# Optimization experiments

Hardware: AMD Instinct MI355X
Metric: run time of the kernel (lower is better)

## Reference

```python
import jax, jax.numpy as jnp
import numpy as np

B, S, D = 2, 1024, 2048      # batch, seq_len, hidden
H, HD = 16, 128              # heads, head_dim
FF = 8192                    # SwiGLU intermediate
R = 3                        # num_recursion
NEG = -1e9                   # additive mask fill (finfo.min analogue)
TEMP, ALPHA = 1.0, 1.0


def _rmsnorm(x, w, eps=1e-6):
    return x * jax.lax.rsqrt(jnp.mean(x * x, axis=-1, keepdims=True) + eps) * w


def _rot_half(x):
    x1, x2 = jnp.split(x, 2, axis=-1)
    return jnp.concatenate([-x2, x1], axis=-1)


def _block(x, cos, sin, sel, ln1, ln2, Wq, Wk, Wv, Wo, Wg, Wu, Wd):
    # Llama decoder layer restricted to selected tokens.
    # The torch code gathers selected tokens + their rows/cols of the 4D causal
    # mask + their RoPE embeddings, runs dense attention on the packed subset,
    # then scatters back. That is mathematically identical to dense attention
    # over the full sequence where keys are masked to selected tokens and only
    # selected-query outputs are kept (RoPE uses ORIGINAL positions in both).
    b, s, d = x.shape
    h = _rmsnorm(x, ln1)
    q = (h @ Wq).reshape(b, s, H, HD)
    k = (h @ Wk).reshape(b, s, H, HD)
    v = (h @ Wv).reshape(b, s, H, HD)
    cs = cos[None, :, None, :]
    sn = sin[None, :, None, :]
    q = q * cs + _rot_half(q) * sn
    k = k * cs + _rot_half(k) * sn
    scores = jnp.einsum('bqhd,bkhd->bhqk', q, k) / np.float32(np.sqrt(HD))
    causal = jnp.tril(jnp.ones((s, s), dtype=bool))
    allowed = causal[None, None, :, :] & sel[:, None, None, :]  # key must be selected
    attn = jax.nn.softmax(jnp.where(allowed, scores, NEG), axis=-1)
    o = jnp.einsum('bhqk,bkhd->bqhd', attn, v).reshape(b, s, d) @ Wo
    x = x + o
    h2 = _rmsnorm(x, ln2)
    return x + (jax.nn.silu(h2 @ Wg) * (h2 @ Wu)) @ Wd


def setup_inputs() -> dict:
    key = jax.random.key(0)
    ks = jax.random.split(key, 9)
    x = jax.random.normal(ks[0], (B, S, D), dtype=jnp.float32)
    # RoPE tables at original positions (what position_embeddings carries)
    inv_freq = 1.0 / (10000.0 ** (np.arange(0, HD, 2, dtype=np.float32) / HD))
    freqs = np.outer(np.arange(S, dtype=np.float32), inv_freq)
    emb = np.concatenate([freqs, freqs], axis=-1)
    cos = jnp.asarray(np.cos(emb), dtype=jnp.float32)
    sin = jnp.asarray(np.sin(emb), dtype=jnp.float32)
    sc = 0.02
    p = lambda k, shp: jax.random.normal(k, shp, dtype=jnp.float32) * sc
    return dict(
        x=x, cos=cos, sin=sin,
        w_router=p(ks[1], (D, R)),
        ln1=jnp.ones((D,), dtype=jnp.float32),
        ln2=jnp.ones((D,), dtype=jnp.float32),
        Wq=p(ks[2], (D, D)), Wk=p(ks[3], (D, D)),
        Wv=p(ks[4], (D, D)), Wo=p(ks[5], (D, D)),
        Wg=p(ks[6], (D, FF)), Wu=p(ks[7], (D, FF)), Wd=p(ks[8], (FF, D)),
    )


def reference(x, cos, sin, w_router, ln1, ln2, Wq, Wk, Wv, Wo, Wg, Wu, Wd):
    # token-level MoR routing: top-1 depth per token, token at depth r is
    # processed by blocks 0..r and its (weighted) output at depth r is final.
    probs = jax.nn.softmax((x / TEMP) @ w_router, axis=-1) * ALPHA  # [B,S,R]
    top_idx = jnp.argmax(probs, axis=-1)                            # [B,S]
    w = jnp.take_along_axis(probs, top_idx[..., None], axis=-1)     # [B,S,1]
    final_x = x
    cur = x
    for index in range(R):
        sel = top_idx >= index                                      # tokens still active
        out = _block(cur, cos, sin, sel, ln1, ln2, Wq, Wk, Wv, Wo, Wg, Wu, Wd)
        fin = (top_idx == index)[..., None]
        final_x = jnp.where(fin, out * w, final_x)                  # finished: scatter weighted
        cur = jnp.where(sel[..., None], out, cur)                   # continuing: update state
    return final_x
```

## Files before the change

### kernel.cpp

```cpp
#include <hip/hip_runtime.h>
#include <hip/hip_bf16.h>

#define B_  2
#define S_  1024
#define D_  2048
#define H_  16
#define HD_ 128
#define FF_ 8192
#define R_  3
#define T_  (B_*S_)

typedef __attribute__((ext_vector_type(8))) short bf16x8;
typedef __attribute__((ext_vector_type(4))) float f32x4;
using bf16 = __hip_bfloat16;

__device__ __forceinline__ float bf2f(short s) {
    return __uint_as_float(((unsigned)(unsigned short)s) << 16);
}
__device__ __forceinline__ unsigned f2bf_bits(float f) {
    bf16 h = __float2bfloat16(f);
    unsigned short u; __builtin_memcpy(&u, &h, 2);
    return (unsigned)u;
}
__device__ __forceinline__ unsigned pack2(float a, float b) {
    return f2bf_bits(a) | (f2bf_bits(b) << 16);
}
__device__ __forceinline__ float wsum(float v) {
    #pragma unroll
    for (int m = 32; m; m >>= 1) v += __shfl_xor(v, m);
    return v;
}
__device__ __forceinline__ void load_lds16(const void* g, void* l) {
    __builtin_amdgcn_global_load_lds((const __attribute__((address_space(1))) void*)g,
                                     (__attribute__((address_space(3))) void*)l, 16, 0, 0);
}

__global__ __launch_bounds__(256)
void transpose_cast(const float* __restrict__ W, bf16* __restrict__ Wt, int K, int N) {
    __shared__ float tile[32][33];
    const int n0 = blockIdx.x * 32, k0 = blockIdx.y * 32;
    const int c = threadIdx.x & 31, r8 = threadIdx.x >> 5;
    #pragma unroll
    for (int i = 0; i < 4; i++) {
        int r = r8 + i * 8;
        tile[r][c] = W[(long)(k0 + r) * N + n0 + c];
    }
    __syncthreads();
    #pragma unroll
    for (int i = 0; i < 4; i++) {
        int r = r8 + i * 8;
        Wt[(long)(n0 + r) * K + k0 + c] = __float2bfloat16(tile[c][r]);
    }
}

__global__ __launch_bounds__(256)
void router_k(const float* __restrict__ X, const float* __restrict__ Wr,
              int* __restrict__ top, float* __restrict__ wsel) {
    const int t = blockIdx.x * 4 + (threadIdx.x >> 6);
    const int lane = threadIdx.x & 63;
    const float* x = X + (long)t * D_;
    float a0 = 0.f, a1 = 0.f, a2 = 0.f;
    for (int j = lane; j < D_; j += 64) {
        float xv = x[j];
        a0 += xv * Wr[j * 3 + 0];
        a1 += xv * Wr[j * 3 + 1];
        a2 += xv * Wr[j * 3 + 2];
    }
    a0 = wsum(a0); a1 = wsum(a1); a2 = wsum(a2);
    if (lane == 0) {
        int arg = 0; float bm = a0;
        if (a1 > bm) { bm = a1; arg = 1; }
        if (a2 > bm) { bm = a2; arg = 2; }
        float s = expf(a0 - bm) + expf(a1 - bm) + expf(a2 - bm);
        top[t]  = arg;
        wsel[t] = 1.0f / s;
    }
}

__global__ __launch_bounds__(256)
void rmsnorm_k(const float* __restrict__ X, const float* __restrict__ G, bf16* __restrict__ Hb) {
    const int t = blockIdx.x, tid = threadIdx.x;
    const float4* xr = (const float4*)(X + (long)t * D_);
    float4 v0 = xr[tid], v1 = xr[tid + 256];
    float ss = v0.x*v0.x + v0.y*v0.y + v0.z*v0.z + v0.w*v0.w
             + v1.x*v1.x + v1.y*v1.y + v1.z*v1.z + v1.w*v1.w;
    ss = wsum(ss);
    __shared__ float red[4];
    if ((tid & 63) == 0) red[tid >> 6] = ss;
    __syncthreads();
    const float r = rsqrtf((red[0] + red[1] + red[2] + red[3]) * (1.0f / D_) + 1e-6f);
    const float4* gr = (const float4*)G;
    float4 g0 = gr[tid], g1 = gr[tid + 256];
    uint2* ob = (uint2*)(Hb + (long)t * D_);
    uint2 o;
    o.x = pack2(v0.x * r * g0.x, v0.y * r * g0.y);
    o.y = pack2(v0.z * r * g0.z, v0.w * r * g0.w);
    ob[tid] = o;
    o.x = pack2(v1.x * r * g1.x, v1.y * r * g1.y);
    o.y = pack2(v1.z * r * g1.z, v1.w * r * g1.w);
    ob[tid + 256] = o;
}

__global__ __launch_bounds__(256)
void rope_k(bf16* __restrict__ q, bf16* __restrict__ k,
            const float* __restrict__ cosb, const float* __restrict__ sinb) {
    const int idx = blockIdx.x * 256 + threadIdx.x;
    const int d = idx & 63;
    const int h = (idx >> 6) & (H_ - 1);
    const int t = idx >> 10;
    const int s = t & (S_ - 1);
    const long base = (long)t * D_ + h * HD_;
    const float c1 = cosb[s * HD_ + d],      s1 = sinb[s * HD_ + d];
    const float c2 = cosb[s * HD_ + d + 64], s2 = sinb[s * HD_ + d + 64];
    float q1 = __bfloat162float(q[base + d]), q2 = __bfloat162float(q[base + d + 64]);
    q[base + d]      = __float2bfloat16(q1 * c1 - q2 * s1);
    q[base + d + 64] = __float2bfloat16(q2 * c2 + q1 * s2);
    float k1 = __bfloat162float(k[base + d]), k2 = __bfloat162float(k[base + d + 64]);
    k[base + d]      = __float2bfloat16(k1 * c1 - k2 * s1);
    k[base + d + 64] = __float2bfloat16(k2 * c2 + k1 * s2);
}

__global__ __launch_bounds__(256)
void attn_k(const bf16* __restrict__ qb, const bf16* __restrict__ kb, const bf16* __restrict__ vb,
            const int* __restrict__ top, int rec, bf16* __restrict__ aob) {
    __shared__ bf16 Ks[64 * 128];
    __shared__ unsigned Vt[128 * 32];
    __shared__ unsigned short Pt[4][64 * 16];
    const int tid = threadIdx.x, w = tid >> 6, lane = tid & 63;
    const int l15 = lane & 15, lg = lane >> 4;
    const int q0 = blockIdx.x * 64;
    const int h = blockIdx.y, b = blockIdx.z;
    const int qw = q0 + w * 16;

    bf16x8 Qf[4];
    {
        const bf16* qptr = qb + ((long)((b * S_ + qw + l15) * H_ + h)) * HD_ + lg * 8;
        #pragma unroll
        for (int ds = 0; ds < 4; ds++) Qf[ds] = *(const bf16x8*)(qptr + ds * 32);
    }

    f32x4 oacc[8] = {};
    float mrow[4] = {-1e30f, -1e30f, -1e30f, -1e30f};
    float lrow[4] = {0.f, 0.f, 0.f, 0.f};
    const float rs = 0.088388347648318447f;
    const int bsrc = (l15 >> 2) << 4;
    const int jj = l15 & 3;

    const int nch = blockIdx.x + 1;
    for (int kc = 0; kc < nch; kc++) {
        __syncthreads();
        #pragma unroll
        for (int i = 0; i < 4; i++) {
            int r = w * 16 + i * 4 + lg;
            int key = kc * 64 + r;
            const bf16* src = kb + ((long)((b * S_ + key) * H_ + h)) * HD_ + ((l15 ^ (r & 7)) * 8);
            load_lds16(src, &Ks[(w * 16 + i * 4) * 128]);
        }
        #pragma unroll
        for (int i = 0; i < 2; i++) {
            int j = i * 256 + tid;
            int c = j & 15, r2 = (j >> 4) & 31;
            long gv = ((long)((b * S_ + kc * 64 + 2 * r2) * H_ + h)) * HD_ + c * 8;
            uint4 va = *(const uint4*)&vb[gv];
            uint4 vbn = *(const uint4*)&vb[gv + D_];
            const unsigned short* pa = (const unsigned short*)&va;
            const unsigned short* pb = (const unsigned short*)&vbn;
            #pragma unroll
            for (int e = 0; e < 8; e++) {
                int d = c * 8 + e;
                int sw = (d ^ (d >> 3)) & 7;
                Vt[d * 32 + (((r2 >> 2) ^ sw) << 2) + (r2 & 3)] =
                    (unsigned)pa[e] | ((unsigned)pb[e] << 16);
            }
        }
        __syncthreads();

        f32x4 sacc[4] = {};
        #pragma unroll
        for (int kg = 0; kg < 4; kg++) {
            const int row = kg * 16 + l15;
            #pragma unroll
            for (int ds = 0; ds < 4; ds++) {
                bf16x8 kf = *(const bf16x8*)&Ks[row * 128 + (((ds * 4 + lg) ^ (row & 7)) * 8)];
                sacc[kg] = __builtin_amdgcn_mfma_f32_16x16x32_bf16(Qf[ds], kf, sacc[kg], 0, 0, 0);
            }
        }

        int selm[4];
        #pragma unroll
        for (int kg = 0; kg < 4; kg++) {
            int key = kc * 64 + kg * 16 + l15;
            selm[kg] = (top[b * S_ + key] >= rec) ? (key) : (1 << 30);
        }
        float pmat[4][4];
        #pragma unroll
        for (int kg = 0; kg < 4; kg++) {
            #pragma unroll
            for (int j = 0; j < 4; j++) {
                float s = sacc[kg][j] * rs;
                pmat[kg][j] = (selm[kg] <= qw + lg * 4 + j) ? s : -1e9f;
            }
        }
        float scj[4];
        #pragma unroll
        for (int j = 0; j < 4; j++) {
            float tm = fmaxf(fmaxf(pmat[0][j], pmat[1][j]), fmaxf(pmat[2][j], pmat[3][j]));
            #pragma unroll
            for (int m = 1; m < 16; m <<= 1) tm = fmaxf(tm, __shfl_xor(tm, m));
            float mnew = fmaxf(mrow[j], tm);
            scj[j] = __expf(mrow[j] - mnew);
            mrow[j] = mnew;
            float ps = 0.f;
            #pragma unroll
            for (int kg = 0; kg < 4; kg++) {
                float p = __expf(pmat[kg][j] - mnew);
                pmat[kg][j] = p;
                ps += p;
            }
            #pragma unroll
            for (int m = 1; m < 16; m <<= 1) ps += __shfl_xor(ps, m);
            lrow[j] = lrow[j] * scj[j] + ps;
        }
        #pragma unroll
        for (int kg = 0; kg < 4; kg++) {
            uint2 u;
            u.x = pack2(pmat[kg][0], pmat[kg][1]);
            u.y = pack2(pmat[kg][2], pmat[kg][3]);
            *(uint2*)&Pt[w][(kg * 16 + l15) * 16 + lg * 4] = u;
        }
        {
            float t0 = __shfl(scj[0], bsrc), t1 = __shfl(scj[1], bsrc);
            float t2 = __shfl(scj[2], bsrc), t3 = __shfl(scj[3], bsrc);
            float scq = (jj == 0) ? t0 : (jj == 1) ? t1 : (jj == 2) ? t2 : t3;
            #pragma unroll
            for (int dg = 0; dg < 8; dg++) {
                oacc[dg][0] *= scq; oacc[dg][1] *= scq;
                oacc[dg][2] *= scq; oacc[dg][3] *= scq;
            }
        }
        #pragma unroll
        for (int ks = 0; ks < 2; ks++) {
            bf16x8 pf;
            #pragma unroll
            for (int e = 0; e < 8; e++)
                pf[e] = (short)Pt[w][(ks * 32 + lg * 8 + e) * 16 + l15];
            #pragma unroll
            for (int dg = 0; dg < 8; dg++) {
                int d = dg * 16 + l15;
                int sw = (d ^ (d >> 3)) & 7;
                bf16x8 vf = *(const bf16x8*)&Vt[d * 32 + (((ks * 4 + lg) ^ sw) << 2)];
                oacc[dg] = __builtin_amdgcn_mfma_f32_16x16x32_bf16(vf, pf, oacc[dg], 0, 0, 0);
            }
        }
    }
    float u0 = __shfl(lrow[0], bsrc), u1 = __shfl(lrow[1], bsrc);
    float u2 = __shfl(lrow[2], bsrc), u3 = __shfl(lrow[3], bsrc);
    float lq = (jj == 0) ? u0 : (jj == 1) ? u1 : (jj == 2) ? u2 : u3;
    float li = 1.0f / lq;
    const long obase = ((long)((b * S_ + qw + l15) * H_ + h)) * HD_ + lg * 4;
    #pragma unroll
    for (int dg = 0; dg < 8; dg++) {
        #pragma unroll
        for (int jp = 0; jp < 2; jp++) {
            unsigned o = pack2(oacc[dg][jp * 2] * li, oacc[dg][jp * 2 + 1] * li);
            *(unsigned*)&aob[obase + dg * 16 + jp * 2] = o;
        }
    }
}

template<int EP>
__global__ __launch_bounds__(256)
void gemm_k(const bf16* __restrict__ A,
            const bf16* __restrict__ Bt0, const bf16* __restrict__ Bt1, const bf16* __restrict__ Bt2,
            bf16* __restrict__ C0, bf16* __restrict__ C1, bf16* __restrict__ C2,
            const float* __restrict__ resid, float* __restrict__ xout,
            const bf16* __restrict__ uaux, bf16* __restrict__ taux,
            const int* __restrict__ topidx, const float* __restrict__ wsel,
            float* __restrict__ finalp, float* __restrict__ curp, int rec,
            int N, int K) {
    __shared__ bf16 As[128 * 32];
    __shared__ bf16 Bs[128 * 32];
    const int tid = threadIdx.x;
    const int w = tid >> 6, lane = tid & 63;

    const int gx = gridDim.x;
    const int nwg = gx * gridDim.y;
    const int orig = blockIdx.y * gx + blockIdx.x;
    const int qc = nwg >> 3, rc = nwg & 7;
    const int xcd = orig & 7, loc = orig >> 3;
    const int wg = (xcd < rc ? xcd * (qc + 1) : rc * (qc + 1) + (xcd - rc) * qc) + loc;
    const int m0 = (wg % gx) * 128, n0 = (wg / gx) * 128;

    const bf16* Bt = (blockIdx.z == 0) ? Bt0 : ((blockIdx.z == 1) ? Bt1 : Bt2);
    bf16* Cb       = (blockIdx.z == 0) ? C0  : ((blockIdx.z == 1) ? C1  : C2);

    const int srow = lane >> 2;
    const int scol = (lane & 3) * 8;
    const long gA = (long)(m0 + w * 32 + srow) * K + scol;
    const long gB = (long)(n0 + w * 32 + srow) * K + scol;

    const int wr = w >> 1, wc = w & 1;
    const int fm = lane & 15, kg = lane >> 4;

    f32x4 acc[4][4] = {};

    for (int kt = 0; kt < K; kt += 32) {
        __syncthreads();
        #pragma unroll
        for (int i = 0; i < 2; i++) {
            load_lds16(A  + gA + (long)(16 * i) * K + kt, &As[(w * 32 + 16 * i) * 32]);
            load_lds16(Bt + gB + (long)(16 * i) * K + kt, &Bs[(w * 32 + 16 * i) * 32]);
        }
        __syncthreads();
        bf16x8 af[4], bfr[4];
        #pragma unroll
        for (int mi = 0; mi < 4; mi++)
            af[mi] = *(const bf16x8*)&As[(wr * 64 + mi * 16 + fm) * 32 + kg * 8];
        #pragma unroll
        for (int ni = 0; ni < 4; ni++)
            bfr[ni] = *(const bf16x8*)&Bs[(wc * 64 + ni * 16 + fm) * 32 + kg * 8];
        #pragma unroll
        for (int mi = 0; mi < 4; mi++)
            #pragma unroll
            for (int ni = 0; ni < 4; ni++)
                acc[mi][ni] = __builtin_amdgcn_mfma_f32_16x16x32_bf16(af[mi], bfr[ni], acc[mi][ni], 0, 0, 0);
    }
    #pragma unroll
    for (int mi = 0; mi < 4; mi++) {
        #pragma unroll
        for (int j = 0; j < 4; j++) {
            const int m = m0 + wr * 64 + mi * 16 + kg * 4 + j;
            int   ti = 0; float wv = 0.f;
            if (EP == 3) { ti = topidx[m]; wv = wsel[m]; }
            #pragma unroll
            for (int ni = 0; ni < 4; ni++) {
                const int n = n0 + wc * 64 + ni * 16 + fm;
                const long off = (long)m * N + n;
                float v = acc[mi][ni][j];
                if (EP == 0) {
                    Cb[off] = __float2bfloat16(v);
                } else if (EP == 1) {
                    xout[off] = v + resid[off];
                } else if (EP == 2) {
                    float u = __bfloat162float(uaux[off]);
                    taux[off] = __float2bfloat16(u * v / (1.f + __expf(-v)));
                } else {
                    float o = v + resid[off];
                    if (ti == rec) finalp[off] = o * wv;
                    if (ti >= rec) curp[off] = o;
                }
            }
        }
    }
}

extern "C" void kernel_launch(void* const* d_in, const int* in_sizes, int n_in,
                              void* d_out, int out_size, void* d_ws, size_t ws_size,
                              hipStream_t stream) {
    const float* x    = (const float*)d_in[0];
    const float* cosb = (const float*)d_in[1];
    const float* sinb = (const float*)d_in[2];
    const float* wrt  = (const float*)d_in[3];
    const float* ln1  = (const float*)d_in[4];
    const float* ln2  = (const float*)d_in[5];
    const float* Wq   = (const float*)d_in[6];
    const float* Wk   = (const float*)d_in[7];
    const float* Wv   = (const float*)d_in[8];
    const float* Wo   = (const float*)d_in[9];
    const float* Wg   = (const float*)d_in[10];
    const float* Wu   = (const float*)d_in[11];
    const float* Wd   = (const float*)d_in[12];

    char* p = (char*)d_ws;
    auto take = [&](size_t bytes) -> char* {
        char* r = p; p += (bytes + 255) & ~(size_t)255; return r;
    };
    bf16* WqT = (bf16*)take((size_t)D_ * D_ * 2);
    bf16* WkT = (bf16*)take((size_t)D_ * D_ * 2);
    bf16* WvT = (bf16*)take((size_t)D_ * D_ * 2);
    bf16* WoT = (bf16*)take((size_t)D_ * D_ * 2);
    bf16* WgT = (bf16*)take((size_t)D_ * FF_ * 2);
    bf16* WuT = (bf16*)take((size_t)D_ * FF_ * 2);
    bf16* WdT = (bf16*)take((size_t)D_ * FF_ * 2);
    float* cur  = (float*)take((size_t)T_ * D_ * 4);
    float* xnew = (float*)take((size_t)T_ * D_ * 4);
    bf16*  hb   = (bf16*)take((size_t)T_ * D_ * 2);
    bf16*  qb   = (bf16*)take((size_t)T_ * D_ * 2);
    bf16*  kbuf = (bf16*)take((size_t)T_ * D_ * 2);
    bf16*  vbuf = (bf16*)take((size_t)T_ * D_ * 2);
    bf16*  aob  = (bf16*)take((size_t)T_ * D_ * 2);
    bf16*  ub   = (bf16*)take((size_t)T_ * FF_ * 2);
    int*   top  = (int*)take((size_t)T_ * 4);
    float* wsel = (float*)take((size_t)T_ * 4);
    (void)ws_size; (void)in_sizes; (void)n_in; (void)out_size;

    transpose_cast<<<dim3(D_ / 32, D_ / 32), 256, 0, stream>>>(Wq, WqT, D_, D_);
    transpose_cast<<<dim3(D_ / 32, D_ / 32), 256, 0, stream>>>(Wk, WkT, D_, D_);
    transpose_cast<<<dim3(D_ / 32, D_ / 32), 256, 0, stream>>>(Wv, WvT, D_, D_);
    transpose_cast<<<dim3(D_ / 32, D_ / 32), 256, 0, stream>>>(Wo, WoT, D_, D_);
    transpose_cast<<<dim3(FF_ / 32, D_ / 32), 256, 0, stream>>>(Wg, WgT, D_, FF_);
    transpose_cast<<<dim3(FF_ / 32, D_ / 32), 256, 0, stream>>>(Wu, WuT, D_, FF_);
    transpose_cast<<<dim3(D_ / 32, FF_ / 32), 256, 0, stream>>>(Wd, WdT, FF_, D_);

    router_k<<<T_ / 4, 256, 0, stream>>>(x, wrt, top, wsel);

    const float* cur_in = x;
    for (int rec = 0; rec < R_; rec++) {
        rmsnorm_k<<<T_, 256, 0, stream>>>(cur_in, ln1, hb);
        gemm_k<0><<<dim3(T_ / 128, D_ / 128, 3), 256, 0, stream>>>(
            hb, WqT, WkT, WvT, qb, kbuf, vbuf,
            nullptr, nullptr, nullptr, nullptr, nullptr, nullptr, nullptr, nullptr, 0, D_, D_);
        rope_k<<<(T_ * H_ * 64) / 256, 256, 0, stream>>>(qb, kbuf, cosb, sinb);
        attn_k<<<dim3(S_ / 64, H_, B_), 256, 0, stream>>>(qb, kbuf, vbuf, top, rec, aob);
        gemm_k<1><<<dim3(T_ / 128, D_ / 128, 1), 256, 0, stream>>>(
            aob, WoT, nullptr, nullptr, nullptr, nullptr, nullptr,
            cur_in, xnew, nullptr, nullptr, nullptr, nullptr, nullptr, nullptr, 0, D_, D_);
        rmsnorm_k<<<T_, 256, 0, stream>>>(xnew, ln2, hb);
        gemm_k<0><<<dim3(T_ / 128, FF_ / 128, 1), 256, 0, stream>>>(
            hb, WuT, nullptr, nullptr, ub, nullptr, nullptr,
            nullptr, nullptr, nullptr, nullptr, nullptr, nullptr, nullptr, nullptr, 0, FF_, D_);
        gemm_k<2><<<dim3(T_ / 128, FF_ / 128, 1), 256, 0, stream>>>(
            hb, WgT, nullptr, nullptr, nullptr, nullptr, nullptr,
            nullptr, nullptr, ub, ub, nullptr, nullptr, nullptr, nullptr, 0, FF_, D_);
        gemm_k<3><<<dim3(T_ / 128, D_ / 128, 1), 256, 0, stream>>>(
            ub, WdT, nullptr, nullptr, nullptr, nullptr, nullptr,
            xnew, nullptr, nullptr, nullptr, top, wsel, (float*)d_out, cur, rec, D_, FF_);
        cur_in = cur;
    }
}
```

Measured before the change: 2.220 ms.

## Use 256x256 double-buffered GEMM for FFN with split-K down projection

Adds a 512-thread GEMM kernel with 256x256 output tiles, 64-wide K steps and double-buffered LDS staging. It computes the up and gate projections in a single launch, then applies SwiGLU in a separate elementwise kernel. The down projection is split four ways along K with atomic adds into a zeroed fp32 buffer, followed by a reduce kernel that applies the residual and routing scatter. The aim is more data reuse and better MFMA utilisation on the dominant FFN GEMMs. In exchange it adds extra passes over memory, atomics and roughly 128KB of LDS per block, which limits occupancy. The gate output reuses the dead q/k/v/attention-output buffers as scratch.

New measurement: 1.959 ms. 11.8% less time.

```diff
diff --git a/kernel.cpp b/kernel.cpp
--- a/kernel.cpp
+++ b/kernel.cpp
@@ -274,9 +274,6 @@
             const bf16* __restrict__ Bt0, const bf16* __restrict__ Bt1, const bf16* __restrict__ Bt2,
             bf16* __restrict__ C0, bf16* __restrict__ C1, bf16* __restrict__ C2,
             const float* __restrict__ resid, float* __restrict__ xout,
-            const bf16* __restrict__ uaux, bf16* __restrict__ taux,
-            const int* __restrict__ topidx, const float* __restrict__ wsel,
-            float* __restrict__ finalp, float* __restrict__ curp, int rec,
             int N, int K) {
     __shared__ bf16 As[128 * 32];
     __shared__ bf16 Bs[128 * 32];
@@ -330,28 +327,138 @@
         #pragma unroll
         for (int j = 0; j < 4; j++) {
             const int m = m0 + wr * 64 + mi * 16 + kg * 4 + j;
-            int   ti = 0; float wv = 0.f;
-            if (EP == 3) { ti = topidx[m]; wv = wsel[m]; }
             #pragma unroll
             for (int ni = 0; ni < 4; ni++) {
                 const int n = n0 + wc * 64 + ni * 16 + fm;
                 const long off = (long)m * N + n;
                 float v = acc[mi][ni][j];
-                if (EP == 0) {
-                    Cb[off] = __float2bfloat16(v);
-                } else if (EP == 1) {
-                    xout[off] = v + resid[off];
-                } else if (EP == 2) {
-                    float u = __bfloat162float(uaux[off]);
-                    taux[off] = __float2bfloat16(u * v / (1.f + __expf(-v)));
-                } else {
-                    float o = v + resid[off];
-                    if (ti == rec) finalp[off] = o * wv;
-                    if (ti >= rec) curp[off] = o;
-                }
-            }
-        }
-    }
+                if (EP == 0) Cb[off] = __float2bfloat16(v);
+                else         xout[off] = v + resid[off];
+            }
+        }
+    }
+}
+
+template<int EP>
+__global__ __launch_bounds__(512, 2)
+void gemm256(const bf16* __restrict__ A, int lda,
+             const bf16* __restrict__ Bt0, const bf16* __restrict__ Bt1, int ldb,
+             int N, int kz,
+             bf16* __restrict__ C0, bf16* __restrict__ C1,
+             float* __restrict__ psum) {
+    __shared__ bf16 As[2][256 * 64];
+    __shared__ bf16 Bs[2][256 * 64];
+    const int tid = threadIdx.x;
+    const int w = tid >> 6, lane = tid & 63;
+    const int z = blockIdx.z;
+
+    const int gx = gridDim.x;
+    const int nwg = gx * gridDim.y;
+    const int orig = blockIdx.y * gx + blockIdx.x;
+    const int qc = nwg >> 3, rc = nwg & 7;
+    const int xcd = orig & 7, loc = orig >> 3;
+    const int wg = (xcd < rc ? xcd * (qc + 1) : rc * (qc + 1) + (xcd - rc) * qc) + loc;
+    const int m0 = (wg % gx) * 256, n0 = (wg / gx) * 256;
+
+    const bf16* Bt = (EP == 0) ? (z ? Bt1 : Bt0) : Bt0;
+    const int kBase = (EP == 1) ? z * kz : 0;
+
+    const int wr = w >> 2, wc = w & 3;
+    const int fm = lane & 15, kg = lane >> 4;
+    const int wchunk = tid & ~63;
+
+    f32x4 acc[8][4] = {};
+
+    auto stage = [&](int buf, int kt) {
+        #pragma unroll
+        for (int i = 0; i < 4; i++) {
+            int c = i * 512 + tid;
+            int row = c >> 3, col = (c & 7) * 8;
+            load_lds16(A  + (long)(m0 + row) * lda + kBase + kt + col,
+                       &As[buf][(i * 512 + wchunk) * 8]);
+            load_lds16(Bt + (long)(n0 + row) * ldb + kBase + kt + col,
+                       &Bs[buf][(i * 512 + wchunk) * 8]);
+        }
+    };
+
+    const int nt = kz >> 6;
+    stage(0, 0);
+    __syncthreads();
+    for (int t = 0; t < nt; t++) {
+        const int cur = t & 1;
+        if (t + 1 < nt) stage(cur ^ 1, (t + 1) << 6);
+        #pragma unroll
+        for (int kk = 0; kk < 2; kk++) {
+            bf16x8 af[8], bfr[4];
+            #pragma unroll
+            for (int mi = 0; mi < 8; mi++)
+                af[mi] = *(const bf16x8*)&As[cur][(wr * 128 + mi * 16 + fm) * 64 + kk * 32 + kg * 8];
+            #pragma unroll
+            for (int ni = 0; ni < 4; ni++)
+                bfr[ni] = *(const bf16x8*)&Bs[cur][(wc * 64 + ni * 16 + fm) * 64 + kk * 32 + kg * 8];
+            __builtin_amdgcn_s_setprio(1);
+            #pragma unroll
+            for (int mi = 0; mi < 8; mi++)
+                #pragma unroll
+                for (int ni = 0; ni < 4; ni++)
+                    acc[mi][ni] = __builtin_amdgcn_mfma_f32_16x16x32_bf16(af[mi], bfr[ni], acc[mi][ni], 0, 0, 0);
+            __builtin_amdgcn_s_setprio(0);
+        }
+        __syncthreads();
+    }
+    #pragma unroll
+    for (int mi = 0; mi < 8; mi++) {
+        #pragma unroll
+        for (int j = 0; j < 4; j++) {
+            const int m = m0 + wr * 128 + mi * 16 + kg * 4 + j;
+            #pragma unroll
+            for (int ni = 0; ni < 4; ni++) {
+                const int n = n0 + wc * 64 + ni * 16 + fm;
+                const long off = (long)m * N + n;
+                float v = acc[mi][ni][j];
+                if (EP == 0) (z ? C1 : C0)[off] = __float2bfloat16(v);
+                else         unsafeAtomicAdd(&psum[off], v);
+            }
+        }
+    }
+}
+
+__global__ __launch_bounds__(256)
+void swiglu_k(const bf16* __restrict__ g, bf16* __restrict__ u) {
+    const long i = ((long)blockIdx.x * 256 + threadIdx.x) * 8;
+    bf16x8 gv = *(const bf16x8*)&g[i];
+    bf16x8 uv = *(const bf16x8*)&u[i];
+    uint4 o;
+    unsigned* op = (unsigned*)&o;
+    #pragma unroll
+    for (int p = 0; p < 4; p++) {
+        float g0 = bf2f(gv[p * 2]),     u0 = bf2f(uv[p * 2]);
+        float g1 = bf2f(gv[p * 2 + 1]), u1 = bf2f(uv[p * 2 + 1]);
+        op[p] = pack2(u0 * g0 / (1.f + __expf(-g0)), u1 * g1 / (1.f + __expf(-g1)));
+    }
+    *(uint4*)&u[i] = o;
+}
+
+__global__ __launch_bounds__(256)
+void zero_k(float4* __restrict__ p) {
+    p[(long)blockIdx.x * 256 + threadIdx.x] = make_float4(0.f, 0.f, 0.f, 0.f);
+}
+
+__global__ __launch_bounds__(256)
+void reduce_ep3(const float* __restrict__ psum, const float* __restrict__ resid,
+                const int* __restrict__ top, const float* __restrict__ wsel,
+                float* __restrict__ finalp, float* __restrict__ curp, int rec) {
+    const long i = ((long)blockIdx.x * 256 + threadIdx.x) * 4;
+    const int m = (int)(i >> 11);
+    float4 ps = *(const float4*)&psum[i];
+    float4 rs = *(const float4*)&resid[i];
+    float4 o = make_float4(ps.x + rs.x, ps.y + rs.y, ps.z + rs.z, ps.w + rs.w);
+    const int ti = top[m];
+    if (ti == rec) {
+        const float wv = wsel[m];
+        *(float4*)&finalp[i] = make_float4(o.x * wv, o.y * wv, o.z * wv, o.w * wv);
+    }
+    if (ti >= rec) *(float4*)&curp[i] = o;
 }
 
 extern "C" void kernel_launch(void* const* d_in, const int* in_sizes, int n_in,
@@ -390,8 +497,10 @@
     bf16*  vbuf = (bf16*)take((size_t)T_ * D_ * 2);
     bf16*  aob  = (bf16*)take((size_t)T_ * D_ * 2);
     bf16*  ub   = (bf16*)take((size_t)T_ * FF_ * 2);
+    float* psum = (float*)take((size_t)T_ * D_ * 4);
     int*   top  = (int*)take((size_t)T_ * 4);
     float* wsel = (float*)take((size_t)T_ * 4);
+    bf16*  gb   = qb;
     (void)ws_size; (void)in_sizes; (void)n_in; (void)out_size;
 
     transpose_cast<<<dim3(D_ / 32, D_ / 32), 256, 0, stream>>>(Wq, WqT, D_, D_);
@@ -408,23 +517,20 @@
     for (int rec = 0; rec < R_; rec++) {
         rmsnorm_k<<<T_, 256, 0, stream>>>(cur_in, ln1, hb);
         gemm_k<0><<<dim3(T_ / 128, D_ / 128, 3), 256, 0, stream>>>(
-            hb, WqT, WkT, WvT, qb, kbuf, vbuf,
-            nullptr, nullptr, nullptr, nullptr, nullptr, nullptr, nullptr, nullptr, 0, D_, D_);
+            hb, WqT, WkT, WvT, qb, kbuf, vbuf, nullptr, nullptr, D_, D_);
         rope_k<<<(T_ * H_ * 64) / 256, 256, 0, stream>>>(qb, kbuf, cosb, sinb);
         attn_k<<<dim3(S_ / 64, H_, B_), 256, 0, stream>>>(qb, kbuf, vbuf, top, rec, aob);
         gemm_k<1><<<dim3(T_ / 128, D_ / 128, 1), 256, 0, stream>>>(
-            aob, WoT, nullptr, nullptr, nullptr, nullptr, nullptr,
-            cur_in, xnew, nullptr, nullptr, nullptr, nullptr, nullptr, nullptr, 0, D_, D_);
+            aob, WoT, nullptr, nullptr, nullptr, nullptr, nullptr, cur_in, xnew, D_, D_);
         rmsnorm_k<<<T_, 256, 0, stream>>>(xnew, ln2, hb);
-        gemm_k<0><<<dim3(T_ / 128, FF_ / 128, 1), 256, 0, stream>>>(
-            hb, WuT, nullptr, nullptr, ub, nullptr, nullptr,
-            nullptr, nullptr, nullptr, nullptr, nullptr, nullptr, nullptr, nullptr, 0, FF_, D_);
-        gemm_k<2><<<dim3(T_ / 128, FF_ / 128, 1), 256, 0, stream>>>(
-            hb, WgT, nullptr, nullptr, nullptr, nullptr, nullptr,
-            nullptr, nullptr, ub, ub, nullptr, nullptr, nullptr, nullptr, 0, FF_, D_);
-        gemm_k<3><<<dim3(T_ / 128, D_ / 128, 1), 256, 0, stream>>>(
-            ub, WdT, nullptr, nullptr, nullptr, nullptr, nullptr,
-            xnew, nullptr, nullptr, nullptr, top, wsel, (float*)d_out, cur, rec, D_, FF_);
+        gemm256<0><<<dim3(T_ / 256, FF_ / 256, 2), 512, 0, stream>>>(
+            hb, D_, WuT, WgT, D_, FF_, D_, ub, gb, nullptr);
+        swiglu_k<<<(T_ * FF_) / (256 * 8), 256, 0, stream>>>(gb, ub);
+        zero_k<<<(T_ * D_) / (256 * 4), 256, 0, stream>>>((float4*)psum);
+        gemm256<1><<<dim3(T_ / 256, D_ / 256, 4), 512, 0, stream>>>(
+            ub, FF_, WdT, nullptr, FF_, D_, D_, nullptr, nullptr, psum);
+        reduce_ep3<<<(T_ * D_) / (256 * 4), 256, 0, stream>>>(
+            psum, xnew, top, wsel, (float*)d_out, cur, rec);
         cur_in = cur;
     }
 }
```
